# Optimization experiments

Measured on AMD Instinct MI355X. Metric: run time of the kernel, lower is better.

Reference implementation:

```python
import jax, jax.numpy as jnp
import numpy as np

B, S, C, L = 32, 256, 50, 20   # batch, max_seq_len, char_emb_dim, word_len
F, W = 30, 3                   # filter_num, char_window_size


def setup_inputs() -> dict:
    key = jax.random.key(0)
    k1, k2, k3 = jax.random.split(key, 3)
    char_embeddings_feature = jax.random.normal(k1, (B, S, C, L), dtype=jnp.float32)
    # torch grouped Conv1d weight: [out_ch=C*F, in_ch/groups=1, kernel=W]
    weight = jax.random.normal(k2, (C * F, 1, W), dtype=jnp.float32) * 0.1
    bias = jax.random.normal(k3, (C * F,), dtype=jnp.float32) * 0.1
    return {"char_embeddings_feature": char_embeddings_feature, "weight": weight, "bias": bias}


def reference(char_embeddings_feature, weight, bias):
    b, s, c, l = char_embeddings_feature.shape
    out_ch = weight.shape[0]
    # Fuse the per-position python loop: fold (batch, seq) into one conv batch dim.
    x = char_embeddings_feature.reshape(b * s, c, l)
    # Grouped (depthwise-style) conv: groups == c, each group has F output filters.
    y = jax.lax.conv_general_dilated(
        x, weight,
        window_strides=(1,), padding='VALID',
        dimension_numbers=('NCH', 'OIH', 'NCH'),
        feature_group_count=c,
    )  # [b*s, c*F, l-W+1]
    y = y + bias[None, :, None]
    # max-pool over conv output length, then restore (batch, seq)
    return y.max(axis=2).reshape(b, s, out_ch)
```

## Files before the change

### kernel.cpp

```cpp
#include <hip/hip_runtime.h>

constexpr int Bc = 32;
constexpr int Sc = 256;
constexpr int Cc = 50;
constexpr int Lc = 20;
constexpr int Fc = 30;
constexpr int Wc = 3;
constexpr int OUT_CH   = Cc * Fc;
constexpr int CONV_LEN = Lc - Wc + 1;
constexpr int XSZ      = Cc * Lc;
constexpr int BLOCK    = 256;
constexpr int CH_PER_T = 6;

__global__ __launch_bounds__(BLOCK, 4)
void charcnn_kernel(const float* __restrict__ x,
                    const float* __restrict__ weight,
                    const float* __restrict__ bias,
                    float* __restrict__ out)
{
    __shared__ float xs[XSZ];

    const int bs = blockIdx.x;
    const int t  = threadIdx.x;

    {
        const float4* src = (const float4*)(x + (size_t)bs * XSZ);
        float4*       dst = (float4*)xs;
        if (t < XSZ / 4) dst[t] = src[t];
    }
    __syncthreads();

    if (t >= OUT_CH / CH_PER_T) return;

    const int c = t / 5;

    float v[Lc];
    {
        const float4* rowv = (const float4*)(xs + c * Lc);
        #pragma unroll
        for (int i = 0; i < Lc / 4; ++i) {
            const float4 q = rowv[i];
            v[4*i+0] = q.x; v[4*i+1] = q.y; v[4*i+2] = q.z; v[4*i+3] = q.w;
        }
    }

    float w[CH_PER_T * Wc];
    {
        const float2* wp = (const float2*)(weight + t * (CH_PER_T * Wc));
        #pragma unroll
        for (int i = 0; i < (CH_PER_T * Wc) / 2; ++i) {
            const float2 q = wp[i];
            w[2*i] = q.x; w[2*i+1] = q.y;
        }
    }
    float bb[CH_PER_T];
    {
        const float2* bp = (const float2*)(bias + t * CH_PER_T);
        #pragma unroll
        for (int i = 0; i < CH_PER_T / 2; ++i) {
            const float2 q = bp[i];
            bb[2*i] = q.x; bb[2*i+1] = q.y;
        }
    }

    float res[CH_PER_T];
    #pragma unroll
    for (int j = 0; j < CH_PER_T; ++j) {
        const float w0 = w[3*j + 0];
        const float w1 = w[3*j + 1];
        const float w2 = w[3*j + 2];

        float cv[CONV_LEN];
        #pragma unroll
        for (int p = 0; p < CONV_LEN; ++p)
            cv[p] = fmaf(v[p], w0, fmaf(v[p+1], w1, v[p+2] * w2));

        float m = fmaxf(fmaxf(cv[0], cv[1]), cv[2]);
        #pragma unroll
        for (int p = 3; p + 1 < CONV_LEN; p += 2)
            m = fmaxf(fmaxf(m, cv[p]), cv[p+1]);
        m = fmaxf(m, cv[CONV_LEN - 1]);

        res[j] = m + bb[j];
    }

    float* op = out + (size_t)bs * OUT_CH + t * CH_PER_T;
    #pragma unroll
    for (int i = 0; i < CH_PER_T / 2; ++i)
        ((float2*)op)[i] = make_float2(res[2*i], res[2*i+1]);
}

extern "C" void kernel_launch(void* const* d_in, const int* in_sizes, int n_in,
                              void* d_out, int out_size, void* d_ws, size_t ws_size,
                              hipStream_t stream) {
    const float* x      = (const float*)d_in[0];
    const float* weight = (const float*)d_in[1];
    const float* bias   = (const float*)d_in[2];
    float* out          = (float*)d_out;

    const int nPos = Bc * Sc;
    charcnn_kernel<<<nPos, BLOCK, 0, stream>>>(x, weight, bias, out);
}
```

Measured before the change: 29.09 us.

## Process four positions per block with double-buffered shared-memory prefetch

Each block now handles four consecutive (batch, seq) positions instead of one. It loads the weights and bias into registers once and prefetches the next position's input row into a second shared buffer while computing the current one. This amortises the weight loads and block launch overhead and overlaps global loads with compute. In exchange the grid has fewer blocks, which reduces parallelism and latency hiding across the GPU.

```diff
diff --git a/kernel.cpp b/kernel.cpp
--- a/kernel.cpp
+++ b/kernel.cpp
@@ -11,6 +11,7 @@
 constexpr int XSZ      = Cc * Lc;
 constexpr int BLOCK    = 256;
 constexpr int CH_PER_T = 6;
+constexpr int NP       = 4;
 
 __global__ __launch_bounds__(BLOCK, 4)
 void charcnn_kernel(const float* __restrict__ x,
@@ -18,43 +19,23 @@
                     const float* __restrict__ bias,
                     float* __restrict__ out)
 {
-    __shared__ float xs[XSZ];
+    __shared__ float xs[2][XSZ];
 
-    const int bs = blockIdx.x;
-    const int t  = threadIdx.x;
+    const int t    = threadIdx.x;
+    const int pos0 = blockIdx.x * NP;
 
-    {
-        const float4* src = (const float4*)(x + (size_t)bs * XSZ);
-        float4*       dst = (float4*)xs;
-        if (t < XSZ / 4) dst[t] = src[t];
-    }
-    __syncthreads();
-
-    if (t >= OUT_CH / CH_PER_T) return;
-
-    const int c = t / 5;
-
-    float v[Lc];
-    {
-        const float4* rowv = (const float4*)(xs + c * Lc);
-        #pragma unroll
-        for (int i = 0; i < Lc / 4; ++i) {
-            const float4 q = rowv[i];
-            v[4*i+0] = q.x; v[4*i+1] = q.y; v[4*i+2] = q.z; v[4*i+3] = q.w;
-        }
-    }
+    const bool stager = (t < XSZ / 4);
+    const bool active = (t < OUT_CH / CH_PER_T);
 
     float w[CH_PER_T * Wc];
-    {
+    float bb[CH_PER_T];
+    if (active) {
         const float2* wp = (const float2*)(weight + t * (CH_PER_T * Wc));
         #pragma unroll
         for (int i = 0; i < (CH_PER_T * Wc) / 2; ++i) {
             const float2 q = wp[i];
             w[2*i] = q.x; w[2*i+1] = q.y;
         }
-    }
-    float bb[CH_PER_T];
-    {
         const float2* bp = (const float2*)(bias + t * CH_PER_T);
         #pragma unroll
         for (int i = 0; i < CH_PER_T / 2; ++i) {
@@ -63,31 +44,62 @@
         }
     }
 
-    float res[CH_PER_T];
-    #pragma unroll
-    for (int j = 0; j < CH_PER_T; ++j) {
-        const float w0 = w[3*j + 0];
-        const float w1 = w[3*j + 1];
-        const float w2 = w[3*j + 2];
+    const int c = t / 5;
 
-        float cv[CONV_LEN];
-        #pragma unroll
-        for (int p = 0; p < CONV_LEN; ++p)
-            cv[p] = fmaf(v[p], w0, fmaf(v[p+1], w1, v[p+2] * w2));
+    if (stager)
+        ((float4*)xs[0])[t] = ((const float4*)(x + (size_t)pos0 * XSZ))[t];
 
-        float m = fmaxf(fmaxf(cv[0], cv[1]), cv[2]);
-        #pragma unroll
-        for (int p = 3; p + 1 < CONV_LEN; p += 2)
-            m = fmaxf(fmaxf(m, cv[p]), cv[p+1]);
-        m = fmaxf(m, cv[CONV_LEN - 1]);
+    for (int p = 0; p < NP; ++p) {
+        const int buf = p & 1;
 
-        res[j] = m + bb[j];
+        float4 pre;
+        const bool doPre = stager && (p + 1 < NP);
+        if (doPre)
+            pre = ((const float4*)(x + (size_t)(pos0 + p + 1) * XSZ))[t];
+
+        __syncthreads();
+
+        float res[CH_PER_T];
+        if (active) {
+            float v[Lc];
+            const float4* rowv = (const float4*)(xs[buf] + c * Lc);
+            #pragma unroll
+            for (int i = 0; i < Lc / 4; ++i) {
+                const float4 q = rowv[i];
+                v[4*i+0] = q.x; v[4*i+1] = q.y; v[4*i+2] = q.z; v[4*i+3] = q.w;
+            }
+
+            #pragma unroll
+            for (int j = 0; j < CH_PER_T; ++j) {
+                const float w0 = w[3*j + 0];
+                const float w1 = w[3*j + 1];
+                const float w2 = w[3*j + 2];
+
+                float cv[CONV_LEN];
+                #pragma unroll
+                for (int q = 0; q < CONV_LEN; ++q)
+                    cv[q] = fmaf(v[q], w0, fmaf(v[q+1], w1, v[q+2] * w2));
+
+                float m = fmaxf(fmaxf(cv[0], cv[1]), cv[2]);
+                #pragma unroll
+                for (int q = 3; q + 1 < CONV_LEN; q += 2)
+                    m = fmaxf(fmaxf(m, cv[q]), cv[q+1]);
+                m = fmaxf(m, cv[CONV_LEN - 1]);
+
+                res[j] = m + bb[j];
+            }
+        }
+
+        if (doPre)
+            ((float4*)xs[buf ^ 1])[t] = pre;
+
+        if (active) {
+            float* op = out + (size_t)(pos0 + p) * OUT_CH + t * CH_PER_T;
+            #pragma unroll
+            for (int i = 0; i < CH_PER_T / 2; ++i)
+                ((float2*)op)[i] = make_float2(res[2*i], res[2*i+1]);
+        }
     }
-
-    float* op = out + (size_t)bs * OUT_CH + t * CH_PER_T;
-    #pragma unroll
-    for (int i = 0; i < CH_PER_T / 2; ++i)
-        ((float2*)op)[i] = make_float2(res[2*i], res[2*i+1]);
 }
 
 extern "C" void kernel_launch(void* const* d_in, const int* in_sizes, int n_in,
@@ -98,6 +110,6 @@
     const float* bias   = (const float*)d_in[2];
     float* out          = (float*)d_out;
 
-    const int nPos = Bc * Sc;
-    charcnn_kernel<<<nPos, BLOCK, 0, stream>>>(x, weight, bias, out);
+    const int nBlocks = (Bc * Sc) / NP;
+    charcnn_kernel<<<nBlocks, BLOCK, 0, stream>>>(x, weight, bias, out);
 }
```

Result: faster. 28.05 us (-3.6%).
